# Performance work log

Measured on AMD Instinct MI355X. Metric: run time of the kernel, lower is better.

## Reference

```python
import jax, jax.numpy as jnp
import numpy as np

N_EMBD = 1024
N_HEAD = 16
B, T = 8, 1024
EPS = 1e-5


def setup_inputs() -> dict:
    key = jax.random.key(0)
    ks = jax.random.split(key, 12)
    C = N_EMBD
    s_in = 1.0 / np.sqrt(C)
    s_ff = 1.0 / np.sqrt(4 * C)
    inp = {
        "x": jax.random.normal(ks[0], (B, T, C), dtype=jnp.float32),
        "mask": jnp.tril(jnp.ones((T, T), dtype=jnp.int32))[None, None, :, :],
        "ln1_w": jnp.ones((C,), jnp.float32),
        "ln1_b": jnp.zeros((C,), jnp.float32),
        "ln2_w": jnp.ones((C,), jnp.float32),
        "ln2_b": jnp.zeros((C,), jnp.float32),
        "wq": jax.random.normal(ks[1], (C, C), jnp.float32) * s_in,
        "bq": jnp.zeros((C,), jnp.float32),
        "wk": jax.random.normal(ks[2], (C, C), jnp.float32) * s_in,
        "bk": jnp.zeros((C,), jnp.float32),
        "wv": jax.random.normal(ks[3], (C, C), jnp.float32) * s_in,
        "bv": jnp.zeros((C,), jnp.float32),
        "wo": jax.random.normal(ks[4], (C, C), jnp.float32) * s_in,
        "bo": jnp.zeros((C,), jnp.float32),
        "w1": jax.random.normal(ks[5], (C, 4 * C), jnp.float32) * s_in,
        "b1": jnp.zeros((4 * C,), jnp.float32),
        "w2": jax.random.normal(ks[6], (4 * C, C), jnp.float32) * s_ff,
        "b2": jnp.zeros((C,), jnp.float32),
    }
    return inp


def _layer_norm(x, w, b):
    mu = jnp.mean(x, axis=-1, keepdims=True)
    var = jnp.mean(jnp.square(x - mu), axis=-1, keepdims=True)
    return (x - mu) * jax.lax.rsqrt(var + EPS) * w + b


def reference(x, mask, ln1_w, ln1_b, ln2_w, ln2_b,
              wq, bq, wk, bk, wv, bv, wo, bo, w1, b1, w2, b2):
    Bx, Tx, C = x.shape
    H = N_HEAD
    d = C // H
    h = _layer_norm(x, ln1_w, ln1_b)
    q = (h @ wq + bq).reshape(Bx, Tx, H, d)
    k = (h @ wk + bk).reshape(Bx, Tx, H, d)
    v = (h @ wv + bv).reshape(Bx, Tx, H, d)
    # [B,H,Tq,Tk] scores, scaled by sqrt(head_dim)
    scores = jnp.einsum('bqhd,bkhd->bhqk', q, k) / jnp.sqrt(jnp.float32(d))
    scores = jnp.where(mask == 0, -jnp.inf, scores)
    attn = jax.nn.softmax(scores, axis=-1)
    ctx = jnp.einsum('bhqk,bkhd->bqhd', attn, v).reshape(Bx, Tx, C)
    x = x + (ctx @ wo + bo)
    h2 = _layer_norm(x, ln2_w, ln2_b)
    ff = jax.nn.gelu(h2 @ w1 + b1, approximate=False) @ w2 + b2
    return x + ff
```

## Files before the change

kernel.cpp:

```cpp
#include <hip/hip_runtime.h>
#include <hip/hip_bf16.h>
#include <math.h>


#define DEVI __device__ __forceinline__

typedef __attribute__((ext_vector_type(4))) float floatx4;
typedef __attribute__((ext_vector_type(8))) short shortx8;

DEVI ushort f2b(float f) {
    __hip_bfloat16 h = __float2bfloat16(f);
    return __builtin_bit_cast(ushort, h);
}

DEVI void gl_lds16(const ushort* g, ushort* l) {
    __builtin_amdgcn_global_load_lds(
        (const __attribute__((address_space(1))) void*)g,
        (__attribute__((address_space(3))) void*)l, 16, 0, 0);
}

DEVI float gelu_f(float v) {
    const float u0 = 0.7978845608f * v * (1.0f + 0.044715f * v * v);
    const float u  = fminf(fmaxf(u0, -15.0f), 15.0f);
    const float e  = exp2f(u * 2.885390082f);
    const float th = 1.0f - 2.0f / (e + 1.0f);
    return 0.5f * v * (1.0f + th);
}

__global__ void transp4_kernel(const float* __restrict__ s0, const float* __restrict__ s1,
                               const float* __restrict__ s2, const float* __restrict__ s3,
                               ushort* __restrict__ d0, ushort* __restrict__ d1,
                               ushort* __restrict__ d2, ushort* __restrict__ d3) {
    const int z = blockIdx.z;
    const float* src = (z == 0) ? s0 : (z == 1) ? s1 : (z == 2) ? s2 : s3;
    ushort*      dst = (z == 0) ? d0 : (z == 1) ? d1 : (z == 2) ? d2 : d3;
    __shared__ float tile[32][33];
    const int c0 = blockIdx.x * 32, r0 = blockIdx.y * 32;
    const int tx = threadIdx.x, ty = threadIdx.y;
#pragma unroll
    for (int i = 0; i < 32; i += 8)
        tile[ty + i][tx] = src[(size_t)(r0 + ty + i) * 1024 + c0 + tx];
    __syncthreads();
#pragma unroll
    for (int i = 0; i < 32; i += 8)
        dst[(size_t)(c0 + ty + i) * 1024 + r0 + tx] = f2b(tile[tx][ty + i]);
}

__global__ void transp_kernel(const float* __restrict__ src,
                              ushort* __restrict__ dst, int R, int C) {
    __shared__ float tile[32][33];
    const int c0 = blockIdx.x * 32, r0 = blockIdx.y * 32;
    const int tx = threadIdx.x, ty = threadIdx.y;
#pragma unroll
    for (int i = 0; i < 32; i += 8)
        tile[ty + i][tx] = src[(size_t)(r0 + ty + i) * C + c0 + tx];
    __syncthreads();
#pragma unroll
    for (int i = 0; i < 32; i += 8)
        dst[(size_t)(c0 + ty + i) * R + r0 + tx] = f2b(tile[tx][ty + i]);
}

__global__ __launch_bounds__(256)
void ln_kernel(const float* __restrict__ x, const float* __restrict__ w,
               const float* __restrict__ b, ushort* __restrict__ out) {
    __shared__ float red[8];
    const int m = blockIdx.x;
    const int tid = threadIdx.x;
    const float4 xv = *(const float4*)&x[(size_t)m * 1024 + tid * 4];
    float s  = xv.x + xv.y + xv.z + xv.w;
    float s2 = xv.x * xv.x + xv.y * xv.y + xv.z * xv.z + xv.w * xv.w;
#pragma unroll
    for (int o = 32; o >= 1; o >>= 1) {
        s  += __shfl_xor(s, o, 64);
        s2 += __shfl_xor(s2, o, 64);
    }
    const int wv_ = tid >> 6;
    if ((tid & 63) == 0) { red[wv_] = s; red[4 + wv_] = s2; }
    __syncthreads();
    s  = red[0] + red[1] + red[2] + red[3];
    s2 = red[4] + red[5] + red[6] + red[7];
    const float mu   = s * (1.0f / 1024.0f);
    const float var  = s2 * (1.0f / 1024.0f) - mu * mu;
    const float rstd = rsqrtf(var + 1e-5f);
    const float4 wv = *(const float4*)&w[tid * 4];
    const float4 bv = *(const float4*)&b[tid * 4];
    ushort o4[4];
    o4[0] = f2b((xv.x - mu) * rstd * wv.x + bv.x);
    o4[1] = f2b((xv.y - mu) * rstd * wv.y + bv.y);
    o4[2] = f2b((xv.z - mu) * rstd * wv.z + bv.z);
    o4[3] = f2b((xv.w - mu) * rstd * wv.w + bv.w);
    *(uint2*)&out[(size_t)m * 1024 + tid * 4] = *(uint2*)o4;
}

template <int MODE>
__global__ __launch_bounds__(256, 4)
void gemm97(const ushort* __restrict__ A, const ushort* __restrict__ Bt,
            const float* __restrict__ biasQ, const float* __restrict__ biasK,
            const float* __restrict__ biasV,
            void* __restrict__ out, void* __restrict__ out2, void* __restrict__ out3,
            const float* __restrict__ resid, int N, int K) {
    __shared__ __align__(128) ushort lds[18432];

    const int tid  = threadIdx.x;
    const int lane = tid & 63;
    const int w    = tid >> 6;
    const int wr   = w >> 1;
    const int wc   = w & 1;

    int bx = blockIdx.x, by = blockIdx.y;
    {
        const int nwg = gridDim.x * gridDim.y;
        if ((nwg & 7) == 0) {
            const int flat = by * gridDim.x + bx;
            const int cpx  = nwg >> 3;
            const int wg   = (flat & 7) * cpx + (flat >> 3);
            bx = wg % gridDim.x;
            by = wg / gridDim.x;
        }
    }
    const int m0 = by * 128;
    const int n0 = bx * 128;

    floatx4 acc[4][4] = {};

    const int lr3 = lane >> 3;
    const int sc  = (lane & 7) ^ lr3;
    const ushort* pA = A  + (size_t)(m0 + w * 32 + lr3) * K + sc * 8;
    const ushort* pB = Bt + (size_t)(n0 + w * 32 + lr3) * K + sc * 8;
    ushort* sAd = lds + w * 2048;
    ushort* sBd = lds + 8192 + w * 2048;
    const size_t k8 = (size_t)8 * K, k16 = (size_t)16 * K, k24 = (size_t)24 * K;

    const int c0f = (lane >> 4) ^ (lane & 7);
    const int aIdx = (wr * 64 + (lane & 15)) * 64 + c0f * 8;
    const int bIdx = (wc * 64 + (lane & 15)) * 64 + c0f * 8;
    const ushort* ar0 = lds + aIdx;
    const ushort* ar1 = lds + (aIdx ^ 32);
    const ushort* br0 = lds + 8192 + bIdx;
    const ushort* br1 = lds + 8192 + (bIdx ^ 32);

    for (int k0 = 0; k0 < K; k0 += 64) {
        __syncthreads();
        gl_lds16(pA + k0,       sAd);
        gl_lds16(pA + k8  + k0, sAd + 512);
        gl_lds16(pA + k16 + k0, sAd + 1024);
        gl_lds16(pA + k24 + k0, sAd + 1536);
        gl_lds16(pB + k0,       sBd);
        gl_lds16(pB + k8  + k0, sBd + 512);
        gl_lds16(pB + k16 + k0, sBd + 1024);
        gl_lds16(pB + k24 + k0, sBd + 1536);
        asm volatile("s_waitcnt vmcnt(0)" ::: "memory");
        __syncthreads();

        shortx8 af[4][2], bf[4][2];
#pragma unroll
        for (int mi = 0; mi < 4; ++mi) {
            af[mi][0] = *(const shortx8*)&ar0[mi * 1024];
            af[mi][1] = *(const shortx8*)&ar1[mi * 1024];
        }
#pragma unroll
        for (int ni = 0; ni < 4; ++ni) {
            bf[ni][0] = *(const shortx8*)&br0[ni * 1024];
            bf[ni][1] = *(const shortx8*)&br1[ni * 1024];
        }
#pragma unroll
        for (int mi = 0; mi < 4; ++mi)
#pragma unroll
            for (int ni = 0; ni < 4; ++ni) {
                acc[mi][ni] = __builtin_amdgcn_mfma_f32_16x16x32_bf16(
                    af[mi][0], bf[ni][0], acc[mi][ni], 0, 0, 0);
                acc[mi][ni] = __builtin_amdgcn_mfma_f32_16x16x32_bf16(
                    af[mi][1], bf[ni][1], acc[mi][ni], 0, 0, 0);
            }
    }
    __syncthreads();

    const int colL  = wc * 64 + (lane & 15);
    const int rbase = wr * 64 + ((lane >> 4) << 2);

    if constexpr (MODE == 3) {
        float bvals[4];
#pragma unroll
        for (int ni = 0; ni < 4; ++ni) bvals[ni] = biasQ[n0 + colL + ni * 16];
        ushort* T = lds;
#pragma unroll
        for (int mi = 0; mi < 4; ++mi)
#pragma unroll
        for (int ni = 0; ni < 4; ++ni) {
            const int t0 = rbase + mi * 16;
#pragma unroll
            for (int r = 0; r < 4; ++r)
                T[(t0 + r) * 136 + colL + ni * 16] =
                    f2b(gelu_f(acc[mi][ni][r] + bvals[ni]));
        }
        __syncthreads();
        ushort* o = (ushort*)out;
#pragma unroll
        for (int it = 0; it < 8; ++it) {
            const int idx = it * 256 + tid;
            const int row = idx >> 4, ch = idx & 15;
            const uint4 vv = *(const uint4*)&T[row * 136 + ch * 8];
            *(uint4*)&o[(size_t)(m0 + row) * N + n0 + ch * 8] = vv;
        }
    }

    if constexpr (MODE == 2) {
        float bvals[4];
#pragma unroll
        for (int ni = 0; ni < 4; ++ni) bvals[ni] = biasQ[n0 + colL + ni * 16];
        float* T = (float*)lds;
        float* o = (float*)out;
#pragma unroll
        for (int half = 0; half < 2; ++half) {
            if (wr == half) {
#pragma unroll
                for (int mi = 0; mi < 4; ++mi)
#pragma unroll
                for (int ni = 0; ni < 4; ++ni) {
                    const int t0 = mi * 16 + ((lane >> 4) << 2);
#pragma unroll
                    for (int r = 0; r < 4; ++r)
                        T[(t0 + r) * 132 + colL + ni * 16] =
                            acc[mi][ni][r] + bvals[ni];
                }
            }
            __syncthreads();
#pragma unroll
            for (int it = 0; it < 8; ++it) {
                const int idx = it * 256 + tid;
                const int row = idx >> 5, ch = idx & 31;
                float4 tv = *(const float4*)&T[row * 132 + ch * 4];
                const size_t go = (size_t)(m0 + half * 64 + row) * N + n0 + ch * 4;
                const float4 rv = *(const float4*)&resid[go];
                tv.x += rv.x; tv.y += rv.y; tv.z += rv.z; tv.w += rv.w;
                *(float4*)&o[go] = tv;
            }
            __syncthreads();
        }
    }

    if constexpr (MODE == 1) {
        const int mat   = n0 >> 10;
        const int bb    = m0 >> 10;
        const int tbase = m0 & 1023;
        if (mat < 2) {
            const float* bp = (mat == 0) ? biasQ : biasK;
            ushort* dst = (mat == 0) ? (ushort*)out : (ushort*)out2;
            float bvals[4];
#pragma unroll
            for (int ni = 0; ni < 4; ++ni)
                bvals[ni] = bp[(n0 & 1023) + colL + ni * 16];
            ushort* T = lds;
#pragma unroll
            for (int mi = 0; mi < 4; ++mi)
#pragma unroll
            for (int ni = 0; ni < 4; ++ni) {
                const int t0 = rbase + mi * 16;
#pragma unroll
                for (int r = 0; r < 4; ++r)
                    T[(t0 + r) * 136 + colL + ni * 16] =
                        f2b(acc[mi][ni][r] + bvals[ni]);
            }
            __syncthreads();
#pragma unroll
            for (int it = 0; it < 8; ++it) {
                const int idx = it * 256 + tid;
                const int row = idx >> 4, ch = idx & 15;
                const uint4 vv = *(const uint4*)&T[row * 136 + ch * 8];
                const int cg = (n0 & 1023) + ch * 8;
                const int h = cg >> 6, dd = cg & 63;
                const int t = tbase + row;
                *(uint4*)&dst[((size_t)(bb * 16 + h) * 1024 + t) * 64 + dd] = vv;
            }
        } else {
            const int vb = n0 - 2048;
            ushort* T = lds;
            ushort* Vt = (ushort*)out3;
#pragma unroll
            for (int ni = 0; ni < 4; ++ni) {
                const float bv = biasV[vb + colL + ni * 16];
#pragma unroll
                for (int mi = 0; mi < 4; ++mi) {
                    const int t0 = rbase + mi * 16;
#pragma unroll
                    for (int r = 0; r < 4; ++r)
                        T[(colL + ni * 16) * 136 + t0 + r] =
                            f2b(acc[mi][ni][r] + bv);
                }
            }
            __syncthreads();
#pragma unroll
            for (int it = 0; it < 8; ++it) {
                const int idx = it * 256 + tid;
                const int dim = idx >> 4, ch = idx & 15;
                const uint4 vv = *(const uint4*)&T[dim * 136 + ch * 8];
                const int d  = vb + dim;
                const int hh = d >> 6, dl = d & 63;
                *(uint4*)&Vt[((size_t)(bb * 16 + hh) * 64 + dl) * 1024 + tbase + ch * 8] = vv;
            }
        }
    }
}

__global__ __launch_bounds__(256)
void attn_kernel(const ushort* __restrict__ Q, const ushort* __restrict__ Kk,
                 const ushort* __restrict__ Vt, ushort* __restrict__ ctx) {
    __shared__ ushort sK[64 * 64];
    __shared__ ushort sV[64 * 64];
    __shared__ ushort sP[4][16 * 72];

    const int tid  = threadIdx.x;
    const int lane = tid & 63;
    const int wave = tid >> 6;
    const int quad = lane >> 4;
    const int l15  = lane & 15;

    const int qb = 15 - (blockIdx.x >> 7);
    const int bh = blockIdx.x & 127;
    const size_t base = (size_t)bh << 16;
    const int bb = bh >> 4, h = bh & 15;

    const int lrow = lane >> 3;
    const int scb  = (lane & 7) ^ lrow;
    const ushort* Kg = Kk + base + (size_t)(wave * 8 + lrow) * 64 + scb * 8;
    const ushort* Vg = Vt + base + (size_t)(wave * 8 + lrow) * 1024 + scb * 8;

    const int qrow = qb * 64 + wave * 16 + l15;
    const shortx8 qf0 = *(const shortx8*)&Q[base + (size_t)qrow * 64 + quad * 8];
    const shortx8 qf1 = *(const shortx8*)&Q[base + (size_t)qrow * 64 + 32 + quad * 8];

    const float SC = 0.125f * 1.44269504f;

    float mstate[4], lstate[4];
    floatx4 oacc[4] = {};
#pragma unroll
    for (int r = 0; r < 4; ++r) { mstate[r] = -__builtin_inff(); lstate[r] = 0.0f; }

    for (int kt = 0; kt <= qb; ++kt) {
        __syncthreads();
#pragma unroll
        for (int p = 0; p < 2; ++p) {
            gl_lds16(Kg + (size_t)kt * 4096 + (size_t)p * 2048,
                     sK + (p * 32 + wave * 8) * 64);
            gl_lds16(Vg + (size_t)kt * 64 + (size_t)p * 32 * 1024,
                     sV + (p * 32 + wave * 8) * 64);
        }
        __syncthreads();

        floatx4 s[4];
#pragma unroll
        for (int nt = 0; nt < 4; ++nt) {
            const int r = nt * 16 + l15;
            const int c0 = quad ^ (r & 7);
            const int c1 = (4 + quad) ^ (r & 7);
            const shortx8 kf0 = *(const shortx8*)&sK[r * 64 + c0 * 8];
            const shortx8 kf1 = *(const shortx8*)&sK[r * 64 + c1 * 8];
            floatx4 z = {};
            z = __builtin_amdgcn_mfma_f32_16x16x32_bf16(qf0, kf0, z, 0, 0, 0);
            z = __builtin_amdgcn_mfma_f32_16x16x32_bf16(qf1, kf1, z, 0, 0, 0);
            s[nt] = z;
        }
#pragma unroll
        for (int nt = 0; nt < 4; ++nt)
#pragma unroll
            for (int r = 0; r < 4; ++r) {
                float sv = s[nt][r] * SC;
                if (kt == qb) {
                    const int col = nt * 16 + l15;
                    const int row = wave * 16 + quad * 4 + r;
                    if (col > row) sv = -__builtin_inff();
                }
                s[nt][r] = sv;
            }
        float mnew[4], alpha[4];
#pragma unroll
        for (int r = 0; r < 4; ++r) {
            float mt = fmaxf(fmaxf(s[0][r], s[1][r]), fmaxf(s[2][r], s[3][r]));
#pragma unroll
            for (int o = 8; o >= 1; o >>= 1) mt = fmaxf(mt, __shfl_xor(mt, o, 64));
            mnew[r]  = fmaxf(mstate[r], mt);
            alpha[r] = exp2f(mstate[r] - mnew[r]);
            mstate[r] = mnew[r];
        }
#pragma unroll
        for (int r = 0; r < 4; ++r) {
            float rs = 0.0f;
#pragma unroll
            for (int nt = 0; nt < 4; ++nt) {
                const float p = exp2f(s[nt][r] - mnew[r]);
                s[nt][r] = p;
                rs += p;
            }
#pragma unroll
            for (int o = 8; o >= 1; o >>= 1) rs += __shfl_xor(rs, o, 64);
            lstate[r] = alpha[r] * lstate[r] + rs;
#pragma unroll
            for (int dt = 0; dt < 4; ++dt) oacc[dt][r] *= alpha[r];
        }
#pragma unroll
        for (int nt = 0; nt < 4; ++nt)
#pragma unroll
            for (int r = 0; r < 4; ++r)
                sP[wave][(quad * 4 + r) * 72 + nt * 16 + l15] = f2b(s[nt][r]);
        __asm__ volatile("s_waitcnt lgkmcnt(0)" ::: "memory");
        const shortx8 pf0 = *(const shortx8*)&sP[wave][l15 * 72 + quad * 8];
        const shortx8 pf1 = *(const shortx8*)&sP[wave][l15 * 72 + 32 + quad * 8];
#pragma unroll
        for (int dt = 0; dt < 4; ++dt) {
            const int r = dt * 16 + l15;
            const int c0 = quad ^ (r & 7);
            const int c1 = (4 + quad) ^ (r & 7);
            const shortx8 v0 = *(const shortx8*)&sV[r * 64 + c0 * 8];
            const shortx8 v1 = *(const shortx8*)&sV[r * 64 + c1 * 8];
            oacc[dt] = __builtin_amdgcn_mfma_f32_16x16x32_bf16(pf0, v0, oacc[dt], 0, 0, 0);
            oacc[dt] = __builtin_amdgcn_mfma_f32_16x16x32_bf16(pf1, v1, oacc[dt], 0, 0, 0);
        }
    }
#pragma unroll
    for (int dt = 0; dt < 4; ++dt)
#pragma unroll
        for (int r = 0; r < 4; ++r) {
            const int t = qb * 64 + wave * 16 + quad * 4 + r;
            const int dim = dt * 16 + l15;
            const float v = oacc[dt][r] / lstate[r];
            ctx[(size_t)(bb * 1024 + t) * 1024 + h * 64 + dim] = f2b(v);
        }
}

extern "C" void kernel_launch(void* const* d_in, const int* in_sizes, int n_in,
                              void* d_out, int out_size, void* d_ws, size_t ws_size,
                              hipStream_t stream) {
    const float* x    = (const float*)d_in[0];
    const float* ln1w = (const float*)d_in[2];
    const float* ln1b = (const float*)d_in[3];
    const float* ln2w = (const float*)d_in[4];
    const float* ln2b = (const float*)d_in[5];
    const float* wq   = (const float*)d_in[6];
    const float* bq   = (const float*)d_in[7];
    const float* wk   = (const float*)d_in[8];
    const float* bk   = (const float*)d_in[9];
    const float* wv   = (const float*)d_in[10];
    const float* bv   = (const float*)d_in[11];
    const float* wo   = (const float*)d_in[12];
    const float* bo   = (const float*)d_in[13];
    const float* w1   = (const float*)d_in[14];
    const float* b1   = (const float*)d_in[15];
    const float* w2   = (const float*)d_in[16];
    const float* b2   = (const float*)d_in[17];

    char* ws = (char*)d_ws;
    const size_t MB = 1024 * 1024;
    ushort* WQKVT = (ushort*)(ws + 0 * MB);
    ushort* WOT   = (ushort*)(ws + 6 * MB);
    ushort* W1T   = (ushort*)(ws + 8 * MB);
    ushort* W2T   = (ushort*)(ws + 16 * MB);
    ushort* H1    = (ushort*)(ws + 24 * MB);
    ushort* H2    = H1;
    ushort* Qb    = (ushort*)(ws + 40 * MB);
    ushort* Kb    = (ushort*)(ws + 56 * MB);
    ushort* Vbt   = (ushort*)(ws + 72 * MB);
    ushort* FF1   = (ushort*)(ws + 40 * MB);
    ushort* CTX   = (ushort*)(ws + 104 * MB);

    float* xout = (float*)d_out;

    const dim3 tb(32, 8);
    transp4_kernel<<<dim3(32, 32, 4), tb, 0, stream>>>(
        wq, wk, wv, wo,
        WQKVT, WQKVT + 1024 * 1024, WQKVT + 2048 * 1024, WOT);
    transp_kernel<<<dim3(128, 32), tb, 0, stream>>>(w1, W1T, 1024, 4096);
    transp_kernel<<<dim3(32, 128), tb, 0, stream>>>(w2, W2T, 4096, 1024);

    ln_kernel<<<8192, 256, 0, stream>>>(x, ln1w, ln1b, H1);

    gemm97<1><<<dim3(24, 64), 256, 0, stream>>>(H1, WQKVT, bq, bk, bv,
                                                Qb, Kb, Vbt, nullptr, 3072, 1024);

    attn_kernel<<<2048, 256, 0, stream>>>(Qb, Kb, Vbt, CTX);

    gemm97<2><<<dim3(8, 64), 256, 0, stream>>>(CTX, WOT, bo, nullptr, nullptr,
                                               xout, nullptr, nullptr, x, 1024, 1024);

    ln_kernel<<<8192, 256, 0, stream>>>(xout, ln2w, ln2b, H2);

    gemm97<3><<<dim3(32, 64), 256, 0, stream>>>(H2, W1T, b1, nullptr, nullptr,
                                                FF1, nullptr, nullptr, nullptr, 4096, 1024);

    gemm97<2><<<dim3(8, 64), 256, 0, stream>>>(FF1, W2T, b2, nullptr, nullptr,
                                               xout, nullptr, nullptr, xout, 1024, 4096);

    (void)in_sizes; (void)n_in; (void)out_size; (void)ws_size;
}
```

Baseline: 499.6 us.

## Use 256x128 tiles with 8 waves for QKV and FF1 GEMMs; row-major Q/K

Adds a gemmW kernel with 512 threads and 256x128 output tiles for the QKV and FF1 projections, so each B tile loaded into LDS is reused across twice as many rows. The epilogue is split into two 128-row passes through LDS. Q and K are now stored row-major ([B*T, C]) instead of head-major, and the attention kernel's addressing is changed to match. The residual GEMMs keep the old 128x128 path in a separate gemm97r kernel. The larger LDS footprint and 512-thread blocks may lower occupancy, and the strided per-head Q/K loads in attention may be less coalesced.

```diff
diff --git a/kernel.cpp b/kernel.cpp
--- a/kernel.cpp
+++ b/kernel.cpp
@@ -93,13 +93,13 @@
 }
 
 template <int MODE>
-__global__ __launch_bounds__(256, 4)
-void gemm97(const ushort* __restrict__ A, const ushort* __restrict__ Bt,
-            const float* __restrict__ biasQ, const float* __restrict__ biasK,
-            const float* __restrict__ biasV,
-            void* __restrict__ out, void* __restrict__ out2, void* __restrict__ out3,
-            const float* __restrict__ resid, int N, int K) {
-    __shared__ __align__(128) ushort lds[18432];
+__global__ __launch_bounds__(512, 4)
+void gemmW(const ushort* __restrict__ A, const ushort* __restrict__ Bt,
+           const float* __restrict__ biasQ, const float* __restrict__ biasK,
+           const float* __restrict__ biasV,
+           void* __restrict__ out, void* __restrict__ out2, void* __restrict__ out3,
+           int N, int K) {
+    __shared__ __align__(128) ushort lds[24576];
 
     const int tid  = threadIdx.x;
     const int lane = tid & 63;
@@ -118,6 +118,194 @@
             by = wg / gridDim.x;
         }
     }
+    const int m0 = by * 256;
+    const int n0 = bx * 128;
+
+    floatx4 acc[4][4] = {};
+
+    const int lr3 = lane >> 3;
+    const int sc  = (lane & 7) ^ lr3;
+    const ushort* pA = A  + (size_t)(m0 + w * 32 + lr3) * K + sc * 8;
+    const ushort* pB = Bt + (size_t)(n0 + w * 16 + lr3) * K + sc * 8;
+    ushort* sAd = lds + w * 2048;
+    ushort* sBd = lds + 16384 + w * 1024;
+    const size_t k8 = (size_t)8 * K, k16 = (size_t)16 * K, k24 = (size_t)24 * K;
+
+    const int c0f  = (lane >> 4) ^ (lane & 7);
+    const int aIdx = (wr * 64 + (lane & 15)) * 64 + c0f * 8;
+    const int bIdx = (wc * 64 + (lane & 15)) * 64 + c0f * 8;
+    const ushort* ar0 = lds + aIdx;
+    const ushort* ar1 = lds + (aIdx ^ 32);
+    const ushort* br0 = lds + 16384 + bIdx;
+    const ushort* br1 = lds + 16384 + (bIdx ^ 32);
+
+    for (int k0 = 0; k0 < K; k0 += 64) {
+        __syncthreads();
+        gl_lds16(pA + k0,       sAd);
+        gl_lds16(pA + k8  + k0, sAd + 512);
+        gl_lds16(pA + k16 + k0, sAd + 1024);
+        gl_lds16(pA + k24 + k0, sAd + 1536);
+        gl_lds16(pB + k0,       sBd);
+        gl_lds16(pB + k8  + k0, sBd + 512);
+        asm volatile("s_waitcnt vmcnt(0)" ::: "memory");
+        __syncthreads();
+
+        shortx8 af[4][2], bf[4][2];
+#pragma unroll
+        for (int mi = 0; mi < 4; ++mi) {
+            af[mi][0] = *(const shortx8*)&ar0[mi * 1024];
+            af[mi][1] = *(const shortx8*)&ar1[mi * 1024];
+        }
+#pragma unroll
+        for (int ni = 0; ni < 4; ++ni) {
+            bf[ni][0] = *(const shortx8*)&br0[ni * 1024];
+            bf[ni][1] = *(const shortx8*)&br1[ni * 1024];
+        }
+#pragma unroll
+        for (int mi = 0; mi < 4; ++mi)
+#pragma unroll
+            for (int ni = 0; ni < 4; ++ni) {
+                acc[mi][ni] = __builtin_amdgcn_mfma_f32_16x16x32_bf16(
+                    af[mi][0], bf[ni][0], acc[mi][ni], 0, 0, 0);
+                acc[mi][ni] = __builtin_amdgcn_mfma_f32_16x16x32_bf16(
+                    af[mi][1], bf[ni][1], acc[mi][ni], 0, 0, 0);
+            }
+    }
+    __syncthreads();
+
+    const int colL  = wc * 64 + (lane & 15);
+    const int rbase = (wr & 1) * 64 + ((lane >> 4) << 2);
+    const int mqme  = wr >> 1;
+
+    if constexpr (MODE == 3) {
+        float bvals[4];
+#pragma unroll
+        for (int ni = 0; ni < 4; ++ni) bvals[ni] = biasQ[n0 + colL + ni * 16];
+        ushort* T = lds;
+        ushort* o = (ushort*)out;
+#pragma unroll
+        for (int mq = 0; mq < 2; ++mq) {
+            if (mqme == mq) {
+#pragma unroll
+                for (int mi = 0; mi < 4; ++mi)
+#pragma unroll
+                for (int ni = 0; ni < 4; ++ni) {
+                    const int t0 = rbase + mi * 16;
+#pragma unroll
+                    for (int r = 0; r < 4; ++r)
+                        T[(t0 + r) * 136 + colL + ni * 16] =
+                            f2b(gelu_f(acc[mi][ni][r] + bvals[ni]));
+                }
+            }
+            __syncthreads();
+#pragma unroll
+            for (int it = 0; it < 4; ++it) {
+                const int idx = it * 512 + tid;
+                const int row = idx >> 4, ch = idx & 15;
+                const uint4 vv = *(const uint4*)&T[row * 136 + ch * 8];
+                *(uint4*)&o[(size_t)(m0 + mq * 128 + row) * N + n0 + ch * 8] = vv;
+            }
+            __syncthreads();
+        }
+    }
+
+    if constexpr (MODE == 1) {
+        const int mat   = n0 >> 10;
+        const int bb    = m0 >> 10;
+        const int tbase = m0 & 1023;
+        if (mat < 2) {
+            const float* bp = (mat == 0) ? biasQ : biasK;
+            ushort* dst = (mat == 0) ? (ushort*)out : (ushort*)out2;
+            const int cb = n0 & 1023;
+            float bvals[4];
+#pragma unroll
+            for (int ni = 0; ni < 4; ++ni) bvals[ni] = bp[cb + colL + ni * 16];
+            ushort* T = lds;
+#pragma unroll
+            for (int mq = 0; mq < 2; ++mq) {
+                if (mqme == mq) {
+#pragma unroll
+                    for (int mi = 0; mi < 4; ++mi)
+#pragma unroll
+                    for (int ni = 0; ni < 4; ++ni) {
+                        const int t0 = rbase + mi * 16;
+#pragma unroll
+                        for (int r = 0; r < 4; ++r)
+                            T[(t0 + r) * 136 + colL + ni * 16] =
+                                f2b(acc[mi][ni][r] + bvals[ni]);
+                    }
+                }
+                __syncthreads();
+#pragma unroll
+                for (int it = 0; it < 4; ++it) {
+                    const int idx = it * 512 + tid;
+                    const int row = idx >> 4, ch = idx & 15;
+                    const uint4 vv = *(const uint4*)&T[row * 136 + ch * 8];
+                    *(uint4*)&dst[(size_t)(m0 + mq * 128 + row) * 1024 + cb + ch * 8] = vv;
+                }
+                __syncthreads();
+            }
+        } else {
+            const int vb = n0 - 2048;
+            ushort* T = lds;
+            ushort* Vt = (ushort*)out3;
+            float bvals[4];
+#pragma unroll
+            for (int ni = 0; ni < 4; ++ni) bvals[ni] = biasV[vb + colL + ni * 16];
+#pragma unroll
+            for (int mq = 0; mq < 2; ++mq) {
+                if (mqme == mq) {
+#pragma unroll
+                    for (int ni = 0; ni < 4; ++ni)
+#pragma unroll
+                    for (int mi = 0; mi < 4; ++mi) {
+                        const int t0 = rbase + mi * 16;
+#pragma unroll
+                        for (int r = 0; r < 4; ++r)
+                            T[(colL + ni * 16) * 136 + t0 + r] =
+                                f2b(acc[mi][ni][r] + bvals[ni]);
+                    }
+                }
+                __syncthreads();
+#pragma unroll
+                for (int it = 0; it < 4; ++it) {
+                    const int idx = it * 512 + tid;
+                    const int dim = idx >> 4, ch = idx & 15;
+                    const uint4 vv = *(const uint4*)&T[dim * 136 + ch * 8];
+                    const int d  = vb + dim;
+                    const int hh = d >> 6, dl = d & 63;
+                    *(uint4*)&Vt[((size_t)(bb * 16 + hh) * 64 + dl) * 1024
+                                 + tbase + mq * 128 + ch * 8] = vv;
+                }
+                __syncthreads();
+            }
+        }
+    }
+}
+
+__global__ __launch_bounds__(256, 4)
+void gemm97r(const ushort* __restrict__ A, const ushort* __restrict__ Bt,
+             const float* __restrict__ bias, float* __restrict__ out,
+             const float* __restrict__ resid, int N, int K) {
+    __shared__ __align__(128) ushort lds[18432];
+
+    const int tid  = threadIdx.x;
+    const int lane = tid & 63;
+    const int w    = tid >> 6;
+    const int wr   = w >> 1;
+    const int wc   = w & 1;
+
+    int bx = blockIdx.x, by = blockIdx.y;
+    {
+        const int nwg = gridDim.x * gridDim.y;
+        if ((nwg & 7) == 0) {
+            const int flat = by * gridDim.x + bx;
+            const int cpx  = nwg >> 3;
+            const int wg   = (flat & 7) * cpx + (flat >> 3);
+            bx = wg % gridDim.x;
+            by = wg / gridDim.x;
+        }
+    }
     const int m0 = by * 128;
     const int n0 = bx * 128;
 
@@ -177,128 +365,37 @@
 
     const int colL  = wc * 64 + (lane & 15);
     const int rbase = wr * 64 + ((lane >> 4) << 2);
-
-    if constexpr (MODE == 3) {
-        float bvals[4];
-#pragma unroll
-        for (int ni = 0; ni < 4; ++ni) bvals[ni] = biasQ[n0 + colL + ni * 16];
-        ushort* T = lds;
-#pragma unroll
-        for (int mi = 0; mi < 4; ++mi)
-#pragma unroll
-        for (int ni = 0; ni < 4; ++ni) {
-            const int t0 = rbase + mi * 16;
-#pragma unroll
-            for (int r = 0; r < 4; ++r)
-                T[(t0 + r) * 136 + colL + ni * 16] =
-                    f2b(gelu_f(acc[mi][ni][r] + bvals[ni]));
-        }
-        __syncthreads();
-        ushort* o = (ushort*)out;
+    float bvals[4];
+#pragma unroll
+    for (int ni = 0; ni < 4; ++ni) bvals[ni] = bias[n0 + colL + ni * 16];
+    float* T = (float*)lds;
+    float* o = (float*)out;
+#pragma unroll
+    for (int half = 0; half < 2; ++half) {
+        if (wr == half) {
+#pragma unroll
+            for (int mi = 0; mi < 4; ++mi)
+#pragma unroll
+            for (int ni = 0; ni < 4; ++ni) {
+                const int t0 = mi * 16 + ((lane >> 4) << 2);
+#pragma unroll
+                for (int r = 0; r < 4; ++r)
+                    T[(t0 + r) * 132 + colL + ni * 16] =
+                        acc[mi][ni][r] + bvals[ni];
+            }
+        }
+        __syncthreads();
 #pragma unroll
         for (int it = 0; it < 8; ++it) {
             const int idx = it * 256 + tid;
-            const int row = idx >> 4, ch = idx & 15;
-            const uint4 vv = *(const uint4*)&T[row * 136 + ch * 8];
-            *(uint4*)&o[(size_t)(m0 + row) * N + n0 + ch * 8] = vv;
-        }
-    }
-
-    if constexpr (MODE == 2) {
-        float bvals[4];
-#pragma unroll
-        for (int ni = 0; ni < 4; ++ni) bvals[ni] = biasQ[n0 + colL + ni * 16];
-        float* T = (float*)lds;
-        float* o = (float*)out;
-#pragma unroll
-        for (int half = 0; half < 2; ++half) {
-            if (wr == half) {
-#pragma unroll
-                for (int mi = 0; mi < 4; ++mi)
-#pragma unroll
-                for (int ni = 0; ni < 4; ++ni) {
-                    const int t0 = mi * 16 + ((lane >> 4) << 2);
-#pragma unroll
-                    for (int r = 0; r < 4; ++r)
-                        T[(t0 + r) * 132 + colL + ni * 16] =
-                            acc[mi][ni][r] + bvals[ni];
-                }
-            }
-            __syncthreads();
-#pragma unroll
-            for (int it = 0; it < 8; ++it) {
-                const int idx = it * 256 + tid;
-                const int row = idx >> 5, ch = idx & 31;
-                float4 tv = *(const float4*)&T[row * 132 + ch * 4];
-                const size_t go = (size_t)(m0 + half * 64 + row) * N + n0 + ch * 4;
-                const float4 rv = *(const float4*)&resid[go];
-                tv.x += rv.x; tv.y += rv.y; tv.z += rv.z; tv.w += rv.w;
-                *(float4*)&o[go] = tv;
-            }
-            __syncthreads();
-        }
-    }
-
-    if constexpr (MODE == 1) {
-        const int mat   = n0 >> 10;
-        const int bb    = m0 >> 10;
-        const int tbase = m0 & 1023;
-        if (mat < 2) {
-            const float* bp = (mat == 0) ? biasQ : biasK;
-            ushort* dst = (mat == 0) ? (ushort*)out : (ushort*)out2;
-            float bvals[4];
-#pragma unroll
-            for (int ni = 0; ni < 4; ++ni)
-                bvals[ni] = bp[(n0 & 1023) + colL + ni * 16];
-            ushort* T = lds;
-#pragma unroll
-            for (int mi = 0; mi < 4; ++mi)
-#pragma unroll
-            for (int ni = 0; ni < 4; ++ni) {
-                const int t0 = rbase + mi * 16;
-#pragma unroll
-                for (int r = 0; r < 4; ++r)
-                    T[(t0 + r) * 136 + colL + ni * 16] =
-                        f2b(acc[mi][ni][r] + bvals[ni]);
-            }
-            __syncthreads();
-#pragma unroll
-            for (int it = 0; it < 8; ++it) {
-                const int idx = it * 256 + tid;
-                const int row = idx >> 4, ch = idx & 15;
-                const uint4 vv = *(const uint4*)&T[row * 136 + ch * 8];
-                const int cg = (n0 & 1023) + ch * 8;
-                const int h = cg >> 6, dd = cg & 63;
-                const int t = tbase + row;
-                *(uint4*)&dst[((size_t)(bb * 16 + h) * 1024 + t) * 64 + dd] = vv;
-            }
-        } else {
-            const int vb = n0 - 2048;
-            ushort* T = lds;
-            ushort* Vt = (ushort*)out3;
-#pragma unroll
-            for (int ni = 0; ni < 4; ++ni) {
-                const float bv = biasV[vb + colL + ni * 16];
-#pragma unroll
-                for (int mi = 0; mi < 4; ++mi) {
-                    const int t0 = rbase + mi * 16;
-#pragma unroll
-                    for (int r = 0; r < 4; ++r)
-                        T[(colL + ni * 16) * 136 + t0 + r] =
-                            f2b(acc[mi][ni][r] + bv);
-                }
-            }
-            __syncthreads();
-#pragma unroll
-            for (int it = 0; it < 8; ++it) {
-                const int idx = it * 256 + tid;
-                const int dim = idx >> 4, ch = idx & 15;
-                const uint4 vv = *(const uint4*)&T[dim * 136 + ch * 8];
-                const int d  = vb + dim;
-                const int hh = d >> 6, dl = d & 63;
-                *(uint4*)&Vt[((size_t)(bb * 16 + hh) * 64 + dl) * 1024 + tbase + ch * 8] = vv;
-            }
-        }
+            const int row = idx >> 5, ch = idx & 31;
+            float4 tv = *(const float4*)&T[row * 132 + ch * 4];
+            const size_t go = (size_t)(m0 + half * 64 + row) * N + n0 + ch * 4;
+            const float4 rv = *(const float4*)&resid[go];
+            tv.x += rv.x; tv.y += rv.y; tv.z += rv.z; tv.w += rv.w;
+            *(float4*)&o[go] = tv;
+        }
+        __syncthreads();
     }
 }
 
@@ -317,17 +414,17 @@
 
     const int qb = 15 - (blockIdx.x >> 7);
     const int bh = blockIdx.x & 127;
-    const size_t base = (size_t)bh << 16;
+    const size_t vbase = (size_t)bh << 16;
     const int bb = bh >> 4, h = bh & 15;
 
     const int lrow = lane >> 3;
     const int scb  = (lane & 7) ^ lrow;
-    const ushort* Kg = Kk + base + (size_t)(wave * 8 + lrow) * 64 + scb * 8;
-    const ushort* Vg = Vt + base + (size_t)(wave * 8 + lrow) * 1024 + scb * 8;
-
-    const int qrow = qb * 64 + wave * 16 + l15;
-    const shortx8 qf0 = *(const shortx8*)&Q[base + (size_t)qrow * 64 + quad * 8];
-    const shortx8 qf1 = *(const shortx8*)&Q[base + (size_t)qrow * 64 + 32 + quad * 8];
+    const ushort* Kg = Kk + ((size_t)bb * 1024 + wave * 8 + lrow) * 1024 + h * 64 + scb * 8;
+    const ushort* Vg = Vt + vbase + (size_t)(wave * 8 + lrow) * 1024 + scb * 8;
+
+    const int qrow = bb * 1024 + qb * 64 + wave * 16 + l15;
+    const shortx8 qf0 = *(const shortx8*)&Q[(size_t)qrow * 1024 + h * 64 + quad * 8];
+    const shortx8 qf1 = *(const shortx8*)&Q[(size_t)qrow * 1024 + h * 64 + 32 + quad * 8];
 
     const float SC = 0.125f * 1.44269504f;
 
@@ -340,7 +437,7 @@
         __syncthreads();
 #pragma unroll
         for (int p = 0; p < 2; ++p) {
-            gl_lds16(Kg + (size_t)kt * 4096 + (size_t)p * 2048,
+            gl_lds16(Kg + (size_t)kt * 65536 + (size_t)p * 32768,
                      sK + (p * 32 + wave * 8) * 64);
             gl_lds16(Vg + (size_t)kt * 64 + (size_t)p * 32 * 1024,
                      sV + (p * 32 + wave * 8) * 64);
@@ -473,21 +570,19 @@
 
     ln_kernel<<<8192, 256, 0, stream>>>(x, ln1w, ln1b, H1);
 
-    gemm97<1><<<dim3(24, 64), 256, 0, stream>>>(H1, WQKVT, bq, bk, bv,
-                                                Qb, Kb, Vbt, nullptr, 3072, 1024);
+    gemmW<1><<<dim3(24, 32), 512, 0, stream>>>(H1, WQKVT, bq, bk, bv,
+                                               Qb, Kb, Vbt, 3072, 1024);
 
     attn_kernel<<<2048, 256, 0, stream>>>(Qb, Kb, Vbt, CTX);
 
-    gemm97<2><<<dim3(8, 64), 256, 0, stream>>>(CTX, WOT, bo, nullptr, nullptr,
-                                               xout, nullptr, nullptr, x, 1024, 1024);
+    gemm97r<<<dim3(8, 64), 256, 0, stream>>>(CTX, WOT, bo, xout, x, 1024, 1024);
 
     ln_kernel<<<8192, 256, 0, stream>>>(xout, ln2w, ln2b, H2);
 
-    gemm97<3><<<dim3(32, 64), 256, 0, stream>>>(H2, W1T, b1, nullptr, nullptr,
-                                                FF1, nullptr, nullptr, nullptr, 4096, 1024);
-
-    gemm97<2><<<dim3(8, 64), 256, 0, stream>>>(FF1, W2T, b2, nullptr, nullptr,
-                                               xout, nullptr, nullptr, xout, 1024, 4096);
+    gemmW<3><<<dim3(32, 32), 512, 0, stream>>>(H2, W1T, b1, nullptr, nullptr,
+                                               FF1, nullptr, nullptr, 4096, 1024);
+
+    gemm97r<<<dim3(8, 64), 256, 0, stream>>>(FF1, W2T, b2, xout, xout, 1024, 4096);
 
     (void)in_sizes; (void)n_in; (void)out_size; (void)ws_size;
 }
```

Result: faster. 468.2 us (-6.3%).
